# Optimization experiments

Hardware: AMD Instinct MI355X
Metric: run time of the kernel (lower is better)

## Reference

```python
import jax, jax.numpy as jnp
import numpy as np

BS, QLEN, DIM, H = 2, 2048, 2048, 16
DH = DIM // H


def setup_inputs() -> dict:
    key = jax.random.key(0)
    ks = jax.random.split(key, 10)
    s = 0.02
    return {
        "input": jax.random.normal(ks[0], (BS, QLEN, DIM), jnp.float32),
        "mask": jnp.ones((BS, QLEN), jnp.int32),
        "wq": jax.random.normal(ks[1], (DIM, DIM), jnp.float32) * s,
        "bq": jax.random.normal(ks[2], (DIM,), jnp.float32) * s,
        "wk": jax.random.normal(ks[3], (DIM, DIM), jnp.float32) * s,
        "bk": jax.random.normal(ks[4], (DIM,), jnp.float32) * s,
        "wv": jax.random.normal(ks[5], (DIM, DIM), jnp.float32) * s,
        "bv": jax.random.normal(ks[6], (DIM,), jnp.float32) * s,
        "wo": jax.random.normal(ks[7], (DIM, DIM), jnp.float32) * s,
        "bo": jax.random.normal(ks[8], (DIM,), jnp.float32) * s,
    }


def _shape(x, bs):
    # (bs, len, dim) -> (bs, H, len, DH)
    return x.reshape(bs, -1, H, DH).transpose(0, 2, 1, 3)


def reference(input, mask, wq, bq, wk, bk, wv, bv, wo, bo):
    bs, qlen, dim = input.shape
    # torch Linear: y = x @ W.T + b
    q = _shape(input @ wq.T + bq, bs)  # (bs,H,q,dh)
    k = _shape(input @ wk.T + bk, bs)  # (bs,H,k,dh)
    v = _shape(input @ wv.T + bv, bs)  # (bs,H,k,dh)
    q = q / jnp.sqrt(jnp.asarray(DH, q.dtype))
    scores = jnp.einsum("bhqd,bhkd->bhqk", q, k)
    # mask (bs, klen): positions where mask==0 are masked with -inf
    neg = (mask == 0)[:, None, None, :]  # (bs,1,1,klen)
    scores = jnp.where(neg, -jnp.inf, scores)
    weights = jax.nn.softmax(scores.astype(jnp.float32), axis=-1).astype(scores.dtype)
    # dropout p=0 (eval): identity
    context = jnp.einsum("bhqk,bhkd->bhqd", weights, v)
    context = context.transpose(0, 2, 1, 3).reshape(bs, qlen, dim)
    return context @ wo.T + bo
```

## Files before the change

kernel.cpp:

```cpp
#include <hip/hip_runtime.h>
#include <hip/hip_bf16.h>

#define BS 2
#define QLEN 2048
#define DIM 2048
#define H 16
#define DH 128
#define MTOT (BS*QLEN)

typedef __hip_bfloat16 bf16;
using f32x4 = __attribute__((ext_vector_type(4))) float;
using s16x8 = __attribute__((ext_vector_type(8))) short;

__device__ inline void gload_lds16(const bf16* g, bf16* l) {
    __builtin_amdgcn_global_load_lds(
        (const __attribute__((address_space(1))) void*)g,
        (__attribute__((address_space(3))) void*)l,
        16, 0, 0);
}

__global__ __launch_bounds__(256) void cast_kernel(const float* __restrict__ in,
                                                   bf16* __restrict__ out, int n4) {
    int i = blockIdx.x * 256 + threadIdx.x;
    if (i < n4) {
        float4 v = ((const float4*)in)[i];
        __hip_bfloat162 p0 = __float22bfloat162_rn(make_float2(v.x, v.y));
        __hip_bfloat162 p1 = __float22bfloat162_rn(make_float2(v.z, v.w));
        ((__hip_bfloat162*)out)[2*i]   = p0;
        ((__hip_bfloat162*)out)[2*i+1] = p1;
    }
}

__global__ __launch_bounds__(256) void cast_w4(
    const float* __restrict__ w0, const float* __restrict__ w1,
    const float* __restrict__ w2, const float* __restrict__ w3,
    bf16* o0, bf16* o1, bf16* o2, bf16* o3, int n4)
{
    const float* in; bf16* out;
    switch (blockIdx.y) {
        case 0:  in = w0; out = o0; break;
        case 1:  in = w1; out = o1; break;
        case 2:  in = w2; out = o2; break;
        default: in = w3; out = o3; break;
    }
    int i = blockIdx.x * 256 + threadIdx.x;
    if (i < n4) {
        float4 v = ((const float4*)in)[i];
        __hip_bfloat162 p0 = __float22bfloat162_rn(make_float2(v.x, v.y));
        __hip_bfloat162 p1 = __float22bfloat162_rn(make_float2(v.z, v.w));
        ((__hip_bfloat162*)out)[2*i]   = p0;
        ((__hip_bfloat162*)out)[2*i+1] = p1;
    }
}

__global__ __launch_bounds__(256) void gemm_qkv(
    const bf16* __restrict__ A,
    const bf16* __restrict__ Wq, const bf16* __restrict__ Wk, const bf16* __restrict__ Wv,
    const float* __restrict__ bq, const float* __restrict__ bk, const float* __restrict__ bv,
    bf16* __restrict__ Qo, bf16* __restrict__ Ko, bf16* __restrict__ Vo,
    float qscale)
{
    __shared__ __align__(16) bf16 smem[128*136];
    bf16* As = smem;
    bf16* Bs = smem + 128*32;

    const int z = blockIdx.z;
    const bf16*  B    = (z == 0) ? Wq : (z == 1) ? Wk : Wv;
    const float* bias = (z == 0) ? bq : (z == 1) ? bk : bv;
    const float  scale = (z == 0) ? qscale : 1.0f;

    const int t = threadIdx.x;
    const int lane = t & 63, w = t >> 6;
    const int row16 = lane & 15, quad = lane >> 4;
    const int m0 = blockIdx.y * 128, n0 = blockIdx.x * 128;
    const int mo = (w >> 1) * 64, no = (w & 1) * 64;

    f32x4 acc[4][4];
    for (int i = 0; i < 4; i++)
        for (int j = 0; j < 4; j++)
            acc[i][j] = (f32x4){0.f, 0.f, 0.f, 0.f};

    const int arow = t >> 2;
    const int achunk = (t & 3) * 8;

    for (int kt = 0; kt < DIM; kt += 32) {
        __syncthreads();
        gload_lds16(A + (size_t)(m0 + arow) * DIM + kt + achunk,      &As[arow*32 + achunk]);
        gload_lds16(A + (size_t)(m0 + 64 + arow) * DIM + kt + achunk, &As[(64+arow)*32 + achunk]);
        gload_lds16(B + (size_t)(n0 + arow) * DIM + kt + achunk,      &Bs[arow*32 + achunk]);
        gload_lds16(B + (size_t)(n0 + 64 + arow) * DIM + kt + achunk, &Bs[(64+arow)*32 + achunk]);
        __syncthreads();

        s16x8 af[4], bfr[4];
        for (int mt = 0; mt < 4; mt++)
            af[mt] = *(const s16x8*)&As[(mo + mt*16 + row16)*32 + quad*8];
        for (int nt = 0; nt < 4; nt++)
            bfr[nt] = *(const s16x8*)&Bs[(no + nt*16 + row16)*32 + quad*8];
        for (int mt = 0; mt < 4; mt++)
            for (int nt = 0; nt < 4; nt++)
                acc[mt][nt] = __builtin_amdgcn_mfma_f32_16x16x32_bf16(
                    af[mt], bfr[nt], acc[mt][nt], 0, 0, 0);
    }

    if (z < 2) {
        bf16* out = (z == 0) ? Qo : Ko;
        for (int mt = 0; mt < 4; mt++)
            for (int nt = 0; nt < 4; nt++) {
                int n = n0 + no + nt*16 + row16;
                float bv_ = bias[n];
                for (int r = 0; r < 4; r++) {
                    int m = m0 + mo + mt*16 + quad*4 + r;
                    out[(size_t)m * DIM + n] = __float2bfloat16((acc[mt][nt][r] + bv_) * scale);
                }
            }
    } else {
        __syncthreads();
        bf16* Ts = smem;
        for (int mt = 0; mt < 4; mt++)
            for (int nt = 0; nt < 4; nt++) {
                int nn = no + nt*16 + row16;
                float bv_ = bias[n0 + nn];
                for (int r = 0; r < 4; r++) {
                    int mm = mo + mt*16 + quad*4 + r;
                    Ts[nn*136 + mm] = __float2bfloat16(acc[mt][nt][r] + bv_);
                }
            }
        __syncthreads();
        const int b = m0 >> 11, q0b = m0 & 2047;
        for (int i = 0; i < 8; i++) {
            int chunk = t + i*256;
            int row = chunk >> 4;
            int c16 = chunk & 15;
            s16x8 val = *(const s16x8*)&Ts[row*136 + c16*8];
            *(s16x8*)(Vo + ((size_t)(b*DIM + n0 + row))*QLEN + q0b + c16*8) = val;
        }
    }
}

__global__ __launch_bounds__(256) void gemm_out(
    const bf16* __restrict__ A, const bf16* __restrict__ B,
    const float* __restrict__ bias, float* __restrict__ out)
{
    __shared__ __align__(16) bf16 As[128*32];
    __shared__ __align__(16) bf16 Bs[128*32];

    const int t = threadIdx.x;
    const int lane = t & 63, w = t >> 6;
    const int row16 = lane & 15, quad = lane >> 4;
    const int m0 = blockIdx.y * 128, n0 = blockIdx.x * 128;
    const int mo = (w >> 1) * 64, no = (w & 1) * 64;

    f32x4 acc[4][4];
    for (int i = 0; i < 4; i++)
        for (int j = 0; j < 4; j++)
            acc[i][j] = (f32x4){0.f, 0.f, 0.f, 0.f};

    const int arow = t >> 2;
    const int achunk = (t & 3) * 8;

    for (int kt = 0; kt < DIM; kt += 32) {
        __syncthreads();
        gload_lds16(A + (size_t)(m0 + arow) * DIM + kt + achunk,      &As[arow*32 + achunk]);
        gload_lds16(A + (size_t)(m0 + 64 + arow) * DIM + kt + achunk, &As[(64+arow)*32 + achunk]);
        gload_lds16(B + (size_t)(n0 + arow) * DIM + kt + achunk,      &Bs[arow*32 + achunk]);
        gload_lds16(B + (size_t)(n0 + 64 + arow) * DIM + kt + achunk, &Bs[(64+arow)*32 + achunk]);
        __syncthreads();

        s16x8 af[4], bfr[4];
        for (int mt = 0; mt < 4; mt++)
            af[mt] = *(const s16x8*)&As[(mo + mt*16 + row16)*32 + quad*8];
        for (int nt = 0; nt < 4; nt++)
            bfr[nt] = *(const s16x8*)&Bs[(no + nt*16 + row16)*32 + quad*8];
        for (int mt = 0; mt < 4; mt++)
            for (int nt = 0; nt < 4; nt++)
                acc[mt][nt] = __builtin_amdgcn_mfma_f32_16x16x32_bf16(
                    af[mt], bfr[nt], acc[mt][nt], 0, 0, 0);
    }

    for (int mt = 0; mt < 4; mt++)
        for (int nt = 0; nt < 4; nt++) {
            int n = n0 + no + nt*16 + row16;
            float bv_ = bias[n];
            for (int r = 0; r < 4; r++) {
                int m = m0 + mo + mt*16 + quad*4 + r;
                out[(size_t)m * DIM + n] = acc[mt][nt][r] + bv_;
            }
        }
}

__global__ __launch_bounds__(256, 2) void attn(
    const bf16* __restrict__ Q, const bf16* __restrict__ Kb,
    const bf16* __restrict__ Vt, const int* __restrict__ mask,
    bf16* __restrict__ Ctx)
{
    __shared__ __align__(16) bf16 Ks[64*128];
    __shared__ __align__(16) bf16 Vs[128*64];
    __shared__ __align__(16) bf16 Pl[4][32*72];

    const int t = threadIdx.x, w = t >> 6, lane = t & 63;
    const int row16 = lane & 15, quad = lane >> 4;
    const int bh = blockIdx.y, b = bh >> 4, h = bh & 15;
    const int q0 = blockIdx.x * 128 + w * 32;

    s16x8 qf[2][4];
    for (int qs = 0; qs < 2; qs++) {
        const bf16* qp = Q + (size_t)(b*QLEN + q0 + qs*16 + row16) * DIM + h*DH;
        for (int ks = 0; ks < 4; ks++)
            qf[qs][ks] = *(const s16x8*)(qp + ks*32 + quad*8);
    }

    f32x4 o[2][8];
    for (int qs = 0; qs < 2; qs++)
        for (int i = 0; i < 8; i++) o[qs][i] = (f32x4){0.f, 0.f, 0.f, 0.f};
    float lsum[2][4] = {{0.f,0.f,0.f,0.f},{0.f,0.f,0.f,0.f}};
    const int* mrow = mask + b * QLEN;

    const bf16* Kbase = Kb + (size_t)b*QLEN*DIM + h*DH;
    const bf16* Vbase = Vt + ((size_t)b*DIM + h*DH) * QLEN;

    for (int kt = 0; kt < QLEN; kt += 64) {
        __syncthreads();
        #pragma unroll
        for (int i = 0; i < 4; i++) {
            int idx = (w*4 + i)*64 + lane;
            int kr = idx >> 4, kc = idx & 15;
            int kg = kc ^ (kr & 15);
            gload_lds16(Kbase + (size_t)(kt + kr) * DIM + kg*8, &Ks[idx*8]);
            int vd = idx >> 3, vc = idx & 7;
            int vg = vc ^ (vd & 7);
            gload_lds16(Vbase + (size_t)vd * QLEN + kt + vg*8, &Vs[idx*8]);
        }
        __syncthreads();

        f32x4 sc[2][4];
        for (int qs = 0; qs < 2; qs++)
            for (int nt = 0; nt < 4; nt++) sc[qs][nt] = (f32x4){0.f, 0.f, 0.f, 0.f};
        #pragma unroll
        for (int ks = 0; ks < 4; ks++) {
            #pragma unroll
            for (int nt = 0; nt < 4; nt++) {
                int rrow = nt*16 + row16;
                int c = (ks*4 + quad) ^ row16;
                s16x8 kf = *(const s16x8*)&Ks[rrow*128 + c*8];
                sc[0][nt] = __builtin_amdgcn_mfma_f32_16x16x32_bf16(qf[0][ks], kf, sc[0][nt], 0, 0, 0);
                sc[1][nt] = __builtin_amdgcn_mfma_f32_16x16x32_bf16(qf[1][ks], kf, sc[1][nt], 0, 0, 0);
            }
        }

        float mval[4];
        #pragma unroll
        for (int nt = 0; nt < 4; nt++)
            mval[nt] = (mrow[kt + nt*16 + row16] != 0) ? -20.0f : -1e30f;

        #pragma unroll
        for (int qs = 0; qs < 2; qs++) {
            #pragma unroll
            for (int r = 0; r < 4; r++) {
                float ts = 0.f;
                #pragma unroll
                for (int nt = 0; nt < 4; nt++) {
                    float p = exp2f(sc[qs][nt][r] + mval[nt]);
                    ts += p;
                    Pl[w][(qs*16 + quad*4 + r)*72 + nt*16 + row16] = __float2bfloat16(p);
                }
                lsum[qs][r] += ts;
            }
        }

        #pragma unroll
        for (int kc = 0; kc < 2; kc++) {
            s16x8 pf0 = *(const s16x8*)&Pl[w][(0*16 + row16)*72 + kc*32 + quad*8];
            s16x8 pf1 = *(const s16x8*)&Pl[w][(1*16 + row16)*72 + kc*32 + quad*8];
            #pragma unroll
            for (int nt = 0; nt < 8; nt++) {
                int d = nt*16 + row16;
                int c = (kc*4 + quad) ^ (d & 7);
                s16x8 vf = *(const s16x8*)&Vs[d*64 + c*8];
                o[0][nt] = __builtin_amdgcn_mfma_f32_16x16x32_bf16(pf0, vf, o[0][nt], 0, 0, 0);
                o[1][nt] = __builtin_amdgcn_mfma_f32_16x16x32_bf16(pf1, vf, o[1][nt], 0, 0, 0);
            }
        }
    }

    for (int qs = 0; qs < 2; qs++) {
        float inv[4];
        for (int r = 0; r < 4; r++) {
            float ts = lsum[qs][r];
            ts += __shfl_xor(ts, 1);
            ts += __shfl_xor(ts, 2);
            ts += __shfl_xor(ts, 4);
            ts += __shfl_xor(ts, 8);
            inv[r] = 1.0f / ts;
        }
        for (int nt = 0; nt < 8; nt++)
            for (int r = 0; r < 4; r++) {
                float v = o[qs][nt][r] * inv[r];
                Ctx[(size_t)(b*QLEN + q0 + qs*16 + quad*4 + r) * DIM + h*DH + nt*16 + row16] =
                    __float2bfloat16(v);
            }
    }
}

extern "C" void kernel_launch(void* const* d_in, const int* in_sizes, int n_in,
                              void* d_out, int out_size, void* d_ws, size_t ws_size,
                              hipStream_t stream) {
    const float* x    = (const float*)d_in[0];
    const int*   mask = (const int*)d_in[1];
    const float* wq   = (const float*)d_in[2];
    const float* bq   = (const float*)d_in[3];
    const float* wk   = (const float*)d_in[4];
    const float* bk   = (const float*)d_in[5];
    const float* wv   = (const float*)d_in[6];
    const float* bv   = (const float*)d_in[7];
    const float* wo   = (const float*)d_in[8];
    const float* bo   = (const float*)d_in[9];

    char* ws = (char*)d_ws;
    const size_t MB = 1024 * 1024;
    bf16* Xb  = (bf16*)(ws);
    bf16* Qb  = (bf16*)(ws + 16*MB);
    bf16* Kb  = (bf16*)(ws + 32*MB);
    bf16* Vtb = (bf16*)(ws + 48*MB);
    bf16* Wqb = (bf16*)(ws + 64*MB);
    bf16* Wkb = (bf16*)(ws + 72*MB);
    bf16* Wvb = (bf16*)(ws + 80*MB);
    bf16* Wob = (bf16*)(ws + 88*MB);
    bf16* Ctx = Xb;

    int n4x = (BS*QLEN*DIM) / 4;
    int n4w = (DIM*DIM) / 4;
    cast_kernel<<<dim3(n4x/256), 256, 0, stream>>>(x, Xb, n4x);
    cast_w4<<<dim3(n4w/256, 4), 256, 0, stream>>>(wq, wk, wv, wo, Wqb, Wkb, Wvb, Wob, n4w);

    const float qscale = 0.08838834764831845f * 1.4426950408889634f;
    gemm_qkv<<<dim3(DIM/128, MTOT/128, 3), 256, 0, stream>>>(
        Xb, Wqb, Wkb, Wvb, bq, bk, bv, Qb, Kb, Vtb, qscale);

    attn<<<dim3(QLEN/128, BS*H), 256, 0, stream>>>(Qb, Kb, Vtb, mask, Ctx);

    gemm_out<<<dim3(DIM/128, MTOT/128), 256, 0, stream>>>(Ctx, Wob, bo, (float*)d_out);
}
```

Baseline: 424.4 us.

## Double-buffer attention K tiles, widen GEMM K-step with swizzled LDS, merge casts

```diff
diff --git a/kernel.cpp b/kernel.cpp
--- a/kernel.cpp
+++ b/kernel.cpp
@@ -19,29 +19,20 @@
         16, 0, 0);
 }
 
-__global__ __launch_bounds__(256) void cast_kernel(const float* __restrict__ in,
-                                                   bf16* __restrict__ out, int n4) {
-    int i = blockIdx.x * 256 + threadIdx.x;
-    if (i < n4) {
-        float4 v = ((const float4*)in)[i];
-        __hip_bfloat162 p0 = __float22bfloat162_rn(make_float2(v.x, v.y));
-        __hip_bfloat162 p1 = __float22bfloat162_rn(make_float2(v.z, v.w));
-        ((__hip_bfloat162*)out)[2*i]   = p0;
-        ((__hip_bfloat162*)out)[2*i+1] = p1;
-    }
-}
-
-__global__ __launch_bounds__(256) void cast_w4(
+__global__ __launch_bounds__(256) void cast6(
+    const float* __restrict__ x,
     const float* __restrict__ w0, const float* __restrict__ w1,
     const float* __restrict__ w2, const float* __restrict__ w3,
-    bf16* o0, bf16* o1, bf16* o2, bf16* o3, int n4)
+    bf16* xo, bf16* o0, bf16* o1, bf16* o2, bf16* o3, int n4)
 {
     const float* in; bf16* out;
     switch (blockIdx.y) {
         case 0:  in = w0; out = o0; break;
         case 1:  in = w1; out = o1; break;
         case 2:  in = w2; out = o2; break;
-        default: in = w3; out = o3; break;
+        case 3:  in = w3; out = o3; break;
+        case 4:  in = x;        out = xo;        break;
+        default: in = x + 4*(size_t)n4; out = xo + 4*(size_t)n4; break;
     }
     int i = blockIdx.x * 256 + threadIdx.x;
     if (i < n4) {
@@ -62,7 +53,7 @@
 {
     __shared__ __align__(16) bf16 smem[128*136];
     bf16* As = smem;
-    bf16* Bs = smem + 128*32;
+    bf16* Bs = smem + 128*64;
 
     const int z = blockIdx.z;
     const bf16*  B    = (z == 0) ? Wq : (z == 1) ? Wk : Wv;
@@ -80,26 +71,34 @@
         for (int j = 0; j < 4; j++)
             acc[i][j] = (f32x4){0.f, 0.f, 0.f, 0.f};
 
-    const int arow = t >> 2;
-    const int achunk = (t & 3) * 8;
-
-    for (int kt = 0; kt < DIM; kt += 32) {
-        __syncthreads();
-        gload_lds16(A + (size_t)(m0 + arow) * DIM + kt + achunk,      &As[arow*32 + achunk]);
-        gload_lds16(A + (size_t)(m0 + 64 + arow) * DIM + kt + achunk, &As[(64+arow)*32 + achunk]);
-        gload_lds16(B + (size_t)(n0 + arow) * DIM + kt + achunk,      &Bs[arow*32 + achunk]);
-        gload_lds16(B + (size_t)(n0 + 64 + arow) * DIM + kt + achunk, &Bs[(64+arow)*32 + achunk]);
-        __syncthreads();
-
-        s16x8 af[4], bfr[4];
-        for (int mt = 0; mt < 4; mt++)
-            af[mt] = *(const s16x8*)&As[(mo + mt*16 + row16)*32 + quad*8];
-        for (int nt = 0; nt < 4; nt++)
-            bfr[nt] = *(const s16x8*)&Bs[(no + nt*16 + row16)*32 + quad*8];
-        for (int mt = 0; mt < 4; mt++)
+    for (int kt = 0; kt < DIM; kt += 64) {
+        __syncthreads();
+        #pragma unroll
+        for (int i = 0; i < 4; i++) {
+            int idx = i*256 + t;
+            int row = idx >> 3, g = idx & 7;
+            int src = g ^ (row & 7);
+            gload_lds16(A + (size_t)(m0 + row) * DIM + kt + src*8, &As[idx*8]);
+            gload_lds16(B + (size_t)(n0 + row) * DIM + kt + src*8, &Bs[idx*8]);
+        }
+        __syncthreads();
+
+        #pragma unroll
+        for (int kh = 0; kh < 2; kh++) {
+            s16x8 af[4], bfr[4];
+            #pragma unroll
+            for (int mt = 0; mt < 4; mt++)
+                af[mt] = *(const s16x8*)&As[(mo + mt*16 + row16)*64 + (((kh*4+quad) ^ (row16&7)))*8];
+            #pragma unroll
             for (int nt = 0; nt < 4; nt++)
-                acc[mt][nt] = __builtin_amdgcn_mfma_f32_16x16x32_bf16(
-                    af[mt], bfr[nt], acc[mt][nt], 0, 0, 0);
+                bfr[nt] = *(const s16x8*)&Bs[(no + nt*16 + row16)*64 + (((kh*4+quad) ^ (row16&7)))*8];
+            #pragma unroll
+            for (int mt = 0; mt < 4; mt++)
+                #pragma unroll
+                for (int nt = 0; nt < 4; nt++)
+                    acc[mt][nt] = __builtin_amdgcn_mfma_f32_16x16x32_bf16(
+                        af[mt], bfr[nt], acc[mt][nt], 0, 0, 0);
+        }
     }
 
     if (z < 2) {
@@ -141,8 +140,8 @@
     const bf16* __restrict__ A, const bf16* __restrict__ B,
     const float* __restrict__ bias, float* __restrict__ out)
 {
-    __shared__ __align__(16) bf16 As[128*32];
-    __shared__ __align__(16) bf16 Bs[128*32];
+    __shared__ __align__(16) bf16 As[128*64];
+    __shared__ __align__(16) bf16 Bs[128*64];
 
     const int t = threadIdx.x;
     const int lane = t & 63, w = t >> 6;
@@ -155,26 +154,34 @@
         for (int j = 0; j < 4; j++)
             acc[i][j] = (f32x4){0.f, 0.f, 0.f, 0.f};
 
-    const int arow = t >> 2;
-    const int achunk = (t & 3) * 8;
-
-    for (int kt = 0; kt < DIM; kt += 32) {
-        __syncthreads();
-        gload_lds16(A + (size_t)(m0 + arow) * DIM + kt + achunk,      &As[arow*32 + achunk]);
-        gload_lds16(A + (size_t)(m0 + 64 + arow) * DIM + kt + achunk, &As[(64+arow)*32 + achunk]);
-        gload_lds16(B + (size_t)(n0 + arow) * DIM + kt + achunk,      &Bs[arow*32 + achunk]);
-        gload_lds16(B + (size_t)(n0 + 64 + arow) * DIM + kt + achunk, &Bs[(64+arow)*32 + achunk]);
-        __syncthreads();
-
-        s16x8 af[4], bfr[4];
-        for (int mt = 0; mt < 4; mt++)
-            af[mt] = *(const s16x8*)&As[(mo + mt*16 + row16)*32 + quad*8];
-        for (int nt = 0; nt < 4; nt++)
-            bfr[nt] = *(const s16x8*)&Bs[(no + nt*16 + row16)*32 + quad*8];
-        for (int mt = 0; mt < 4; mt++)
+    for (int kt = 0; kt < DIM; kt += 64) {
+        __syncthreads();
+        #pragma unroll
+        for (int i = 0; i < 4; i++) {
+            int idx = i*256 + t;
+            int row = idx >> 3, g = idx & 7;
+            int src = g ^ (row & 7);
+            gload_lds16(A + (size_t)(m0 + row) * DIM + kt + src*8, &As[idx*8]);
+            gload_lds16(B + (size_t)(n0 + row) * DIM + kt + src*8, &Bs[idx*8]);
+        }
+        __syncthreads();
+
+        #pragma unroll
+        for (int kh = 0; kh < 2; kh++) {
+            s16x8 af[4], bfr[4];
+            #pragma unroll
+            for (int mt = 0; mt < 4; mt++)
+                af[mt] = *(const s16x8*)&As[(mo + mt*16 + row16)*64 + (((kh*4+quad) ^ (row16&7)))*8];
+            #pragma unroll
             for (int nt = 0; nt < 4; nt++)
-                acc[mt][nt] = __builtin_amdgcn_mfma_f32_16x16x32_bf16(
-                    af[mt], bfr[nt], acc[mt][nt], 0, 0, 0);
+                bfr[nt] = *(const s16x8*)&Bs[(no + nt*16 + row16)*64 + (((kh*4+quad) ^ (row16&7)))*8];
+            #pragma unroll
+            for (int mt = 0; mt < 4; mt++)
+                #pragma unroll
+                for (int nt = 0; nt < 4; nt++)
+                    acc[mt][nt] = __builtin_amdgcn_mfma_f32_16x16x32_bf16(
+                        af[mt], bfr[nt], acc[mt][nt], 0, 0, 0);
+        }
     }
 
     for (int mt = 0; mt < 4; mt++)
@@ -193,9 +200,9 @@
     const bf16* __restrict__ Vt, const int* __restrict__ mask,
     bf16* __restrict__ Ctx)
 {
-    __shared__ __align__(16) bf16 Ks[64*128];
+    __shared__ __align__(16) bf16 Ks[2][64*128];
     __shared__ __align__(16) bf16 Vs[128*64];
-    __shared__ __align__(16) bf16 Pl[4][32*72];
+    __shared__ __align__(16) bf16 Pl[4][32*64];
 
     const int t = threadIdx.x, w = t >> 6, lane = t & 63;
     const int row16 = lane & 15, quad = lane >> 4;
@@ -218,19 +225,39 @@
     const bf16* Kbase = Kb + (size_t)b*QLEN*DIM + h*DH;
     const bf16* Vbase = Vt + ((size_t)b*DIM + h*DH) * QLEN;
 
-    for (int kt = 0; kt < QLEN; kt += 64) {
-        __syncthreads();
+    #pragma unroll
+    for (int i = 0; i < 4; i++) {
+        int idx = i*256 + t;
+        int kr = idx >> 4, kc = idx & 15;
+        int kg = kc ^ (kr & 15);
+        gload_lds16(Kbase + (size_t)kr * DIM + kg*8, &Ks[0][idx*8]);
+    }
+
+    for (int it = 0; it < QLEN/64; it++) {
+        const int kt = it * 64, buf = it & 1;
+        __syncthreads();
+
+        if (it + 1 < QLEN/64) {
+            #pragma unroll
+            for (int i = 0; i < 4; i++) {
+                int idx = i*256 + t;
+                int kr = idx >> 4, kc = idx & 15;
+                int kg = kc ^ (kr & 15);
+                gload_lds16(Kbase + (size_t)(kt + 64 + kr) * DIM + kg*8, &Ks[buf^1][idx*8]);
+            }
+        }
         #pragma unroll
         for (int i = 0; i < 4; i++) {
-            int idx = (w*4 + i)*64 + lane;
-            int kr = idx >> 4, kc = idx & 15;
-            int kg = kc ^ (kr & 15);
-            gload_lds16(Kbase + (size_t)(kt + kr) * DIM + kg*8, &Ks[idx*8]);
+            int idx = i*256 + t;
             int vd = idx >> 3, vc = idx & 7;
             int vg = vc ^ (vd & 7);
             gload_lds16(Vbase + (size_t)vd * QLEN + kt + vg*8, &Vs[idx*8]);
         }
-        __syncthreads();
+
+        float mval[4];
+        #pragma unroll
+        for (int nt = 0; nt < 4; nt++)
+            mval[nt] = (mrow[kt + nt*16 + row16] != 0) ? -20.0f : -1e30f;
 
         f32x4 sc[2][4];
         for (int qs = 0; qs < 2; qs++)
@@ -241,36 +268,37 @@
             for (int nt = 0; nt < 4; nt++) {
                 int rrow = nt*16 + row16;
                 int c = (ks*4 + quad) ^ row16;
-                s16x8 kf = *(const s16x8*)&Ks[rrow*128 + c*8];
+                s16x8 kf = *(const s16x8*)&Ks[buf][rrow*128 + c*8];
                 sc[0][nt] = __builtin_amdgcn_mfma_f32_16x16x32_bf16(qf[0][ks], kf, sc[0][nt], 0, 0, 0);
                 sc[1][nt] = __builtin_amdgcn_mfma_f32_16x16x32_bf16(qf[1][ks], kf, sc[1][nt], 0, 0, 0);
             }
         }
 
-        float mval[4];
-        #pragma unroll
-        for (int nt = 0; nt < 4; nt++)
-            mval[nt] = (mrow[kt + nt*16 + row16] != 0) ? -20.0f : -1e30f;
-
         #pragma unroll
         for (int qs = 0; qs < 2; qs++) {
             #pragma unroll
             for (int r = 0; r < 4; r++) {
+                int prow = qs*16 + quad*4 + r;
                 float ts = 0.f;
                 #pragma unroll
                 for (int nt = 0; nt < 4; nt++) {
                     float p = exp2f(sc[qs][nt][r] + mval[nt]);
                     ts += p;
-                    Pl[w][(qs*16 + quad*4 + r)*72 + nt*16 + row16] = __float2bfloat16(p);
+                    int chunk = nt*2 + (row16 >> 3);
+                    int slot = chunk ^ (prow & 7);
+                    Pl[w][prow*64 + slot*8 + (row16 & 7)] = __float2bfloat16(p);
                 }
                 lsum[qs][r] += ts;
             }
         }
 
+        __syncthreads();
+
         #pragma unroll
         for (int kc = 0; kc < 2; kc++) {
-            s16x8 pf0 = *(const s16x8*)&Pl[w][(0*16 + row16)*72 + kc*32 + quad*8];
-            s16x8 pf1 = *(const s16x8*)&Pl[w][(1*16 + row16)*72 + kc*32 + quad*8];
+            int pslot0 = ((kc*4 + quad) ^ (row16 & 7));
+            s16x8 pf0 = *(const s16x8*)&Pl[w][(0*16 + row16)*64 + pslot0*8];
+            s16x8 pf1 = *(const s16x8*)&Pl[w][(1*16 + row16)*64 + pslot0*8];
             #pragma unroll
             for (int nt = 0; nt < 8; nt++) {
                 int d = nt*16 + row16;
@@ -327,10 +355,9 @@
     bf16* Wob = (bf16*)(ws + 88*MB);
     bf16* Ctx = Xb;
 
-    int n4x = (BS*QLEN*DIM) / 4;
     int n4w = (DIM*DIM) / 4;
-    cast_kernel<<<dim3(n4x/256), 256, 0, stream>>>(x, Xb, n4x);
-    cast_w4<<<dim3(n4w/256, 4), 256, 0, stream>>>(wq, wk, wv, wo, Wqb, Wkb, Wvb, Wob, n4w);
+    cast6<<<dim3(n4w/256, 6), 256, 0, stream>>>(x, wq, wk, wv, wo,
+                                                Xb, Wqb, Wkb, Wvb, Wob, n4w);
 
     const float qscale = 0.08838834764831845f * 1.4426950408889634f;
     gemm_qkv<<<dim3(DIM/128, MTOT/128, 3), 256, 0, stream>>>(
```

New measurement: 416.1 us. No clear change (-2.0%).
